# Performance work log

Hardware: AMD Instinct MI355X
Metric: run time of the kernel (lower is better)

The kernel has to match this reference:

```python
import jax, jax.numpy as jnp
import numpy as np

B, E, F = 16384, 128, 6
ITEM_V, CATE_V, HIST = 91718, 11, 50
I_IDX, J_IDX = np.triu_indices(F, k=1)  # 15 field pairs, loop order (0,1),(0,2),...
EPS = 1e-5


def _xavier(key, shape):
    fan_in, fan_out = shape[0], shape[-1]
    std = (2.0 / (fan_in + fan_out)) ** 0.5
    return std * jax.random.normal(key, shape, dtype=jnp.float32)


def setup_inputs() -> dict:
    key = jax.random.key(0)
    ks = jax.random.split(key, 20)
    inp = {
        'item_id': jax.random.randint(ks[0], (B,), 0, ITEM_V),
        'item_emb_d128': jax.random.normal(ks[1], (B, 128), dtype=jnp.float32),
        'likes_level': jax.random.randint(ks[2], (B,), 0, CATE_V),
        'views_level': jax.random.randint(ks[3], (B,), 0, CATE_V),
        'item_seq': jax.random.randint(ks[4], (B, HIST), 0, ITEM_V),
        # learned parameters
        'item_emb': 0.05 * jax.random.normal(ks[5], (ITEM_V, E), dtype=jnp.float32),
        'cate_emb': 0.05 * jax.random.normal(ks[6], (CATE_V, E), dtype=jnp.float32),
        'mm_W': _xavier(ks[7], (128, E)), 'mm_b': jnp.zeros((E,), jnp.float32),
        'ln_g': jnp.ones((E,), jnp.float32), 'ln_b': jnp.zeros((E,), jnp.float32),
        'se_W1': _xavier(ks[8], (F, F // 2)), 'se_b1': jnp.zeros((F // 2,), jnp.float32),
        'se_W2': _xavier(ks[9], (F // 2, F)), 'se_b2': jnp.zeros((F,), jnp.float32),
        'bi_W': _xavier(ks[10], (E, E)),
        'mlp_W1': _xavier(ks[11], (21 * E, 512)), 'mlp_b1': jnp.zeros((512,), jnp.float32),
        'bn1_g': jnp.ones((512,), jnp.float32), 'bn1_b': jnp.zeros((512,), jnp.float32),
        'bn1_rm': jnp.zeros((512,), jnp.float32), 'bn1_rv': jnp.ones((512,), jnp.float32),
        'mlp_W2': _xavier(ks[12], (512, 256)), 'mlp_b2': jnp.zeros((256,), jnp.float32),
        'bn2_g': jnp.ones((256,), jnp.float32), 'bn2_b': jnp.zeros((256,), jnp.float32),
        'bn2_rm': jnp.zeros((256,), jnp.float32), 'bn2_rv': jnp.ones((256,), jnp.float32),
        'mlp_W3': _xavier(ks[13], (256, 1)), 'mlp_b3': jnp.zeros((1,), jnp.float32),
    }
    return inp


def _forward(item_id, item_emb_d128, likes_level, views_level, item_seq,
             item_emb, cate_emb, mm_W, mm_b, ln_g, ln_b,
             se_W1, se_b1, se_W2, se_b2, bi_W,
             mlp_W1, mlp_b1, bn1_g, bn1_b, bn1_rm, bn1_rv,
             mlp_W2, mlp_b2, bn2_g, bn2_b, bn2_rm, bn2_rv,
             mlp_W3, mlp_b3):
    b = item_id.shape[0]
    tab = item_emb.at[0].set(0.0)  # padding_idx=0
    like_feat = cate_emb[likes_level]
    view_feat = cate_emb[views_level]
    item_feat = tab[item_id]
    # mm_proj: Linear -> LayerNorm -> ReLU
    mm = item_emb_d128 @ mm_W + mm_b
    mu = mm.mean(-1, keepdims=True)
    var = jnp.var(mm, axis=-1, keepdims=True)
    mm = jax.nn.relu((mm - mu) / jnp.sqrt(var + EPS) * ln_g + ln_b)
    # masked mean pooling over history
    seq_emb = tab[item_seq]                               # (B, HIST, E)
    valid = (item_seq != 0).astype(seq_emb.dtype)
    seq_sum = (seq_emb * valid[..., None]).sum(1)
    cnt = jnp.clip(valid.sum(1, keepdims=True), 1.0)
    hist_feat = seq_sum / cnt
    user_feat = jnp.zeros((b, E), seq_emb.dtype)
    x = jnp.stack([user_feat, like_feat, view_feat, item_feat, mm, hist_feat], axis=1)  # (B,6,E)
    # SENet
    z = x.mean(-1)
    w = jax.nn.sigmoid(jax.nn.relu(z @ se_W1 + se_b1) @ se_W2 + se_b2)
    xs = x * w[:, :, None]
    # bilinear 'all'
    xw = jnp.einsum('bfe,ed->bfd', xs, bi_W)
    p = xs[:, I_IDX, :] * xw[:, J_IDX, :]                 # (B,15,E)
    c = jnp.concatenate([xs.reshape(b, -1), p.reshape(b, -1)], axis=1)  # (B, 2688)
    # MLP head (eval mode: BN uses running stats, dropout off)
    h = c @ mlp_W1 + mlp_b1
    h = jax.nn.relu((h - bn1_rm) / jnp.sqrt(bn1_rv + EPS) * bn1_g + bn1_b)
    h = h @ mlp_W2 + mlp_b2
    h = jax.nn.relu((h - bn2_rm) / jnp.sqrt(bn2_rv + EPS) * bn2_g + bn2_b)
    logits = h @ mlp_W3 + mlp_b3
    return jax.nn.sigmoid(logits)[:, 0]


def reference(item_id, item_emb_d128, likes_level, views_level, item_seq,
              item_emb, cate_emb, mm_W, mm_b, ln_g, ln_b,
              se_W1, se_b1, se_W2, se_b2, bi_W,
              mlp_W1, mlp_b1, bn1_g, bn1_b, bn1_rm, bn1_rv,
              mlp_W2, mlp_b2, bn2_g, bn2_b, bn2_rm, bn2_rv,
              mlp_W3, mlp_b3):
    return _forward(item_id, item_emb_d128, likes_level, views_level, item_seq,
                    item_emb, cate_emb, mm_W, mm_b, ln_g, ln_b,
                    se_W1, se_b1, se_W2, se_b2, bi_W,
                    mlp_W1, mlp_b1, bn1_g, bn1_b, bn1_rm, bn1_rv,
                    mlp_W2, mlp_b2, bn2_g, bn2_b, bn2_rm, bn2_rv,
                    mlp_W3, mlp_b3)
```

## Files before the change

### kernel.cpp

```cpp
#include <hip/hip_runtime.h>
#include <hip/hip_bf16.h>

typedef __hip_bfloat16 bfloat;
typedef __bf16 bf16x8 __attribute__((ext_vector_type(8)));
typedef float f32x4 __attribute__((ext_vector_type(4)));

#define B_SZ   16384
#define E_DIM  128
#define HIST_L 50


#define IPACK 0x3221110000ULL
#define JPACK 0x3323213210ULL

__device__ __forceinline__ void gl_lds16(const void* g, void* l) {
    __builtin_amdgcn_global_load_lds(
        (const __attribute__((address_space(1))) unsigned int*)g,
        (__attribute__((address_space(3))) unsigned int*)l, 16, 0, 0);
}

__device__ __forceinline__ bf16x8 mul_bf16x8(bf16x8 a, bf16x8 b) {
    union { bf16x8 v; __hip_bfloat162 h[4]; } ua, ub, ur;
    ua.v = a; ub.v = b;
    #pragma unroll
    for (int i = 0; i < 4; ++i) ur.h[i] = __hmul2(ua.h[i], ub.h[i]);
    return ur.v;
}

__global__ __launch_bounds__(256) void feat_kernel(
    const int* __restrict__ item_id,
    const int* __restrict__ likes, const int* __restrict__ views,
    const int* __restrict__ seq,
    const float* __restrict__ item_emb, const float* __restrict__ cate_emb,
    const float* __restrict__ mm,
    const float* __restrict__ ln_g, const float* __restrict__ ln_b,
    const float* __restrict__ se_W1, const float* __restrict__ se_b1,
    const float* __restrict__ se_W2, const float* __restrict__ se_b2,
    bfloat* __restrict__ xs)
{
    const int tid = threadIdx.x;
    const int r   = tid >> 7;
    const int e   = tid & 127;
    const int b   = blockIdx.x * 2 + r;
    const int w   = tid >> 6;

    __shared__ float redh[2][4][128];
    __shared__ int   seq_s[2][64];
    __shared__ float lnred[4], lnred2[4];
    __shared__ float zred[5][4];
    __shared__ float wsh[2][6];
    __shared__ int   cnt_s[2];

    if (e < 64) seq_s[r][e] = (e < HIST_L) ? seq[(size_t)b * HIST_L + e] : 0;
    __syncthreads();

    const int iid = item_id[b];
    const float like_v = cate_emb[likes[b] * 128 + e];
    const float view_v = cate_emb[views[b] * 128 + e];
    const float item_raw = item_emb[(size_t)iid * 128 + e];
    const float item_v = iid ? item_raw : 0.f;
    const float acc = mm[(size_t)b * 128 + e];

    const int q   = e >> 5;
    const int l32 = e & 31;
    float4 hs = make_float4(0.f, 0.f, 0.f, 0.f);
    #pragma unroll
    for (int g = 0; g < 13; ++g) {
        int s = seq_s[r][g * 4 + q];
        const float4 v = *(const float4*)&item_emb[(size_t)s * 128 + l32 * 4];
        float m = (s != 0) ? 1.f : 0.f;
        hs.x = fmaf(v.x, m, hs.x);
        hs.y = fmaf(v.y, m, hs.y);
        hs.z = fmaf(v.z, m, hs.z);
        hs.w = fmaf(v.w, m, hs.w);
    }

    {
        float v = acc;
        #pragma unroll
        for (int off = 32; off > 0; off >>= 1) v += __shfl_down(v, off, 64);
        if ((tid & 63) == 0) lnred[w] = v;
    }
    __syncthreads();
    const float mu = (lnred[2 * r] + lnred[2 * r + 1]) * (1.f / 128.f);
    const float d  = acc - mu;
    {
        float v = d * d;
        #pragma unroll
        for (int off = 32; off > 0; off >>= 1) v += __shfl_down(v, off, 64);
        if ((tid & 63) == 0) lnred2[w] = v;
    }
    redh[r][q][l32 * 4 + 0] = hs.x;
    redh[r][q][l32 * 4 + 1] = hs.y;
    redh[r][q][l32 * 4 + 2] = hs.z;
    redh[r][q][l32 * 4 + 3] = hs.w;
    if ((w & 1) == 0 && e < 64) {
        bool valid = (e < HIST_L) && (seq_s[r][e] != 0);
        unsigned long long m = __ballot(valid);
        if (e == 0) cnt_s[r] = (int)__popcll(m);
    }
    __syncthreads();
    const float var = (lnred2[2 * r] + lnred2[2 * r + 1]) * (1.f / 128.f);
    float xmm = d * rsqrtf(var + 1e-5f) * ln_g[e] + ln_b[e];
    xmm = fmaxf(xmm, 0.f);

    const int cnt = cnt_s[r] > 0 ? cnt_s[r] : 1;
    const float hist_v = (redh[r][0][e] + redh[r][1][e] +
                          redh[r][2][e] + redh[r][3][e]) / (float)cnt;

    {
        float s1 = like_v, s2 = view_v, s3 = item_v, s4 = xmm, s5 = hist_v;
        #pragma unroll
        for (int off = 32; off > 0; off >>= 1) {
            s1 += __shfl_down(s1, off, 64);
            s2 += __shfl_down(s2, off, 64);
            s3 += __shfl_down(s3, off, 64);
            s4 += __shfl_down(s4, off, 64);
            s5 += __shfl_down(s5, off, 64);
        }
        if ((tid & 63) == 0) {
            zred[0][w] = s1; zred[1][w] = s2; zred[2][w] = s3;
            zred[3][w] = s4; zred[4][w] = s5;
        }
    }
    __syncthreads();

    if (e == 0) {
        float z[6];
        z[0] = 0.f;
        #pragma unroll
        for (int f = 1; f < 6; ++f)
            z[f] = (zred[f - 1][2 * r] + zred[f - 1][2 * r + 1]) * (1.f / 128.f);
        float a[3];
        #pragma unroll
        for (int j = 0; j < 3; ++j) {
            float s = se_b1[j];
            #pragma unroll
            for (int f = 0; f < 6; ++f) s += z[f] * se_W1[f * 3 + j];
            a[j] = fmaxf(s, 0.f);
        }
        #pragma unroll
        for (int f = 0; f < 6; ++f) {
            float s = se_b2[f];
            #pragma unroll
            for (int j = 0; j < 3; ++j) s += a[j] * se_W2[j * 6 + f];
            wsh[r][f] = 1.f / (1.f + expf(-s));
        }
    }
    __syncthreads();

    bfloat* xrow = xs + (size_t)b * 640;
    xrow[0 * 128 + e] = __float2bfloat16(like_v * wsh[r][1]);
    xrow[1 * 128 + e] = __float2bfloat16(view_v * wsh[r][2]);
    xrow[2 * 128 + e] = __float2bfloat16(item_v * wsh[r][3]);
    xrow[3 * 128 + e] = __float2bfloat16(xmm    * wsh[r][4]);
    xrow[4 * 128 + e] = __float2bfloat16(hist_v * wsh[r][5]);
}

__global__ __launch_bounds__(256) void transpose_f32_bf16(
    const float* __restrict__ in, bfloat* __restrict__ out, int K, int N)
{
    int idx = blockIdx.x * 256 + threadIdx.x;
    if (idx < K * N) {
        int k = idx / N, n = idx % N;
        out[(size_t)n * K + k] = __float2bfloat16(in[idx]);
    }
}

__global__ __launch_bounds__(256) void transpose_W1c(
    const float* __restrict__ W1, bfloat* __restrict__ W1t)
{
    int idx = blockIdx.x * 256 + threadIdx.x;
    if (idx < 512 * 1920) {
        int n = idx / 1920, kk = idx % 1920;
        int orig = kk + (kk < 640 ? 128 : 768);
        W1t[idx] = __float2bfloat16(W1[(size_t)orig * 512 + n]);
    }
}

__global__ __launch_bounds__(256) void cvt_f32_bf16(
    const float* __restrict__ in, bfloat* __restrict__ out, int n8)
{
    int idx = blockIdx.x * 256 + threadIdx.x;
    if (idx < n8) {
        float4 f0 = ((const float4*)in)[idx * 2];
        float4 f1 = ((const float4*)in)[idx * 2 + 1];
        union { bf16x8 v; unsigned short s[8]; } u;
        u.s[0] = __bfloat16_as_ushort(__float2bfloat16(f0.x));
        u.s[1] = __bfloat16_as_ushort(__float2bfloat16(f0.y));
        u.s[2] = __bfloat16_as_ushort(__float2bfloat16(f0.z));
        u.s[3] = __bfloat16_as_ushort(__float2bfloat16(f0.w));
        u.s[4] = __bfloat16_as_ushort(__float2bfloat16(f1.x));
        u.s[5] = __bfloat16_as_ushort(__float2bfloat16(f1.y));
        u.s[6] = __bfloat16_as_ushort(__float2bfloat16(f1.z));
        u.s[7] = __bfloat16_as_ushort(__float2bfloat16(f1.w));
        ((bf16x8*)out)[idx] = u.v;
    }
}

__global__ __launch_bounds__(256) void pair_kernel(
    const bfloat* __restrict__ xs, const bfloat* __restrict__ xw,
    bfloat* __restrict__ P, int total)
{
    int idx = blockIdx.x * 256 + threadIdx.x;
    if (idx >= total) return;
    int b = idx / 160, c = idx % 160;
    int pp = c >> 4, q = c & 15;
    int isl = (int)((IPACK >> (4 * pp)) & 15);
    int jsl = (int)((JPACK >> (4 * pp)) & 15);
    bf16x8 a = *(const bf16x8*)&xs[(size_t)b * 640 + isl * 128 + q * 8];
    bf16x8 w = *(const bf16x8*)&xw[((size_t)b * 4 + jsl) * 128 + q * 8];
    *(bf16x8*)&P[(size_t)b * 1280 + c * 8] = mul_bf16x8(a, w);
}

__global__ __launch_bounds__(256) void bn_pre(
    const float* __restrict__ lb1, const float* __restrict__ g1,
    const float* __restrict__ bb1, const float* __restrict__ rm1,
    const float* __restrict__ rv1,
    const float* __restrict__ lb2, const float* __restrict__ g2,
    const float* __restrict__ bb2, const float* __restrict__ rm2,
    const float* __restrict__ rv2,
    const float* __restrict__ mm_b,
    float* __restrict__ S1, float* __restrict__ T1,
    float* __restrict__ S2, float* __restrict__ T2,
    float* __restrict__ Tmm)
{
    int j = blockIdx.x * 256 + threadIdx.x;
    if (j < 512) {
        float s = g1[j] * rsqrtf(rv1[j] + 1e-5f);
        S1[j] = s;
        T1[j] = (lb1[j] - rm1[j]) * s + bb1[j];
    } else if (j < 768) {
        int k = j - 512;
        float s = g2[k] * rsqrtf(rv2[k] + 1e-5f);
        S2[k] = s;
        T2[k] = (lb2[k] - rm2[k]) * s + bb2[k];
    } else if (j < 896) {
        Tmm[j - 768] = mm_b[j - 768];
    }
}

template<int MODE, int EPI, int F32OUT>
__global__ __launch_bounds__(256) void gemm_bt(
    const void* __restrict__ A, const bfloat* __restrict__ A2,
    const bfloat* __restrict__ Bt, void* __restrict__ C,
    int M, int N, int K,
    const float* __restrict__ S, const float* __restrict__ T)
{
    __shared__ __align__(16) short As[3][64 * 64];
    __shared__ __align__(16) short Bs[3][64 * 64];

    const int tid  = threadIdx.x;
    const int bm   = blockIdx.x * 64;
    const int bn   = blockIdx.y * 64;
    const int wave = tid >> 6;
    const int lane = tid & 63;
    const int wm   = (wave >> 1) * 32;
    const int wn   = (wave & 1) * 32;

    const short* Ag  = (const short*)A;
    const short* A2g = (const short*)A2;
    const short* Bg  = (const short*)Bt;

    f32x4 acc[2][2];
    #pragma unroll
    for (int i = 0; i < 2; ++i)
        #pragma unroll
        for (int j = 0; j < 2; ++j)
            acc[i][j] = (f32x4){0.f, 0.f, 0.f, 0.f};

    const int srow = tid >> 3;
    const int sck  = tid & 7;

    auto stage = [&](int buf, int kt) {
        #pragma unroll
        for (int rr = 0; rr < 2; ++rr) {
            int row = srow + rr * 32;
            int g   = sck ^ (row & 7);
            gl_lds16(&Bg[(long)(bn + row) * K + kt + g * 8],
                     &Bs[buf][row * 64 + sck * 8]);
        }
        #pragma unroll
        for (int rr = 0; rr < 2; ++rr) {
            int row = srow + rr * 32;
            int g   = sck ^ (row & 7);
            const short* src;
            if (MODE == 4) {
                long rb = (long)(bm + row);
                src = (kt < 640)
                    ? &Ag [rb * 640  + kt + g * 8]
                    : &A2g[rb * 1280 + (kt - 640) + g * 8];
            } else if (MODE == 2) {
                int gr = bm + row;
                src = &Ag[((long)(gr >> 2)) * 640 +
                          ((gr & 3) + 1) * 128 + kt + g * 8];
            } else {
                src = &Ag[(long)(bm + row) * K + kt + g * 8];
            }
            gl_lds16(src, &As[buf][row * 64 + sck * 8]);
        }
    };

    const int rbase = lane & 15;
    const int cswz  = rbase & 7;

    const int nk = K >> 6;
    stage(0, 0);
    stage(1, 64);

    for (int i = 0; i < nk; ++i) {
        if (i + 1 < nk) asm volatile("s_waitcnt vmcnt(4)" ::: "memory");
        else            asm volatile("s_waitcnt vmcnt(0)" ::: "memory");
        __builtin_amdgcn_s_barrier();
        __builtin_amdgcn_sched_barrier(0);

        const int cur = i % 3;
        #pragma unroll
        for (int h = 0; h < 2; ++h) {
            const int cg = h * 4 + (lane >> 4);
            const int ca = (cg ^ cswz) << 3;
            bf16x8 af[2], bfr[2];
            #pragma unroll
            for (int mt = 0; mt < 2; ++mt)
                af[mt] = *(const bf16x8*)
                    &As[cur][(wm + mt * 16 + rbase) * 64 + ca];
            #pragma unroll
            for (int nt = 0; nt < 2; ++nt)
                bfr[nt] = *(const bf16x8*)
                    &Bs[cur][(wn + nt * 16 + rbase) * 64 + ca];
            #pragma unroll
            for (int mt = 0; mt < 2; ++mt)
                #pragma unroll
                for (int nt = 0; nt < 2; ++nt)
                    acc[mt][nt] = __builtin_amdgcn_mfma_f32_16x16x32_bf16(
                        af[mt], bfr[nt], acc[mt][nt], 0, 0, 0);
        }

        if (i + 2 < nk) stage((i + 2) % 3, (i + 2) << 6);
    }

    const int col0 = lane & 15;
    const int row0 = (lane >> 4) * 4;
    #pragma unroll
    for (int nt = 0; nt < 2; ++nt) {
        int col = bn + wn + nt * 16 + col0;
        float s = 1.f, t = 0.f;
        if (EPI) { s = (EPI == 1) ? S[col] : 1.f; t = T[col]; }
        #pragma unroll
        for (int mt = 0; mt < 2; ++mt) {
            #pragma unroll
            for (int i = 0; i < 4; ++i) {
                int row = bm + wm + mt * 16 + row0 + i;
                float v = acc[mt][nt][i];
                if (EPI == 1) v = fmaxf(v * s + t, 0.f);
                if (EPI == 2) v = v + t;
                if (F32OUT) ((float*)C)[(size_t)row * N + col] = v;
                else ((bfloat*)C)[(size_t)row * N + col] = __float2bfloat16(v);
            }
        }
    }
}

__global__ __launch_bounds__(256) void head_kernel(
    const bfloat* __restrict__ h2, const float* __restrict__ W3,
    const float* __restrict__ b3, float* __restrict__ out)
{
    int lane = threadIdx.x & 63;
    int row  = blockIdx.x * 4 + (threadIdx.x >> 6);
    float acc = 0.f;
    #pragma unroll
    for (int i = 0; i < 4; ++i)
        acc += __bfloat162float(h2[(size_t)row * 256 + i * 64 + lane]) *
               W3[i * 64 + lane];
    #pragma unroll
    for (int off = 32; off > 0; off >>= 1) acc += __shfl_down(acc, off, 64);
    if (lane == 0) {
        float l = acc + b3[0];
        out[row] = 1.f / (1.f + expf(-l));
    }
}

extern "C" void kernel_launch(void* const* d_in, const int* in_sizes, int n_in,
                              void* d_out, int out_size, void* d_ws, size_t ws_size,
                              hipStream_t stream) {
    const int*   item_id = (const int*)  d_in[0];
    const float* d128    = (const float*)d_in[1];
    const int*   likes   = (const int*)  d_in[2];
    const int*   views   = (const int*)  d_in[3];
    const int*   seq     = (const int*)  d_in[4];
    const float* item_emb= (const float*)d_in[5];
    const float* cate_emb= (const float*)d_in[6];
    const float* mm_W    = (const float*)d_in[7];
    const float* mm_b    = (const float*)d_in[8];
    const float* ln_g    = (const float*)d_in[9];
    const float* ln_b    = (const float*)d_in[10];
    const float* se_W1   = (const float*)d_in[11];
    const float* se_b1   = (const float*)d_in[12];
    const float* se_W2   = (const float*)d_in[13];
    const float* se_b2   = (const float*)d_in[14];
    const float* bi_W    = (const float*)d_in[15];
    const float* W1      = (const float*)d_in[16];
    const float* b1      = (const float*)d_in[17];
    const float* bn1_g   = (const float*)d_in[18];
    const float* bn1_b   = (const float*)d_in[19];
    const float* bn1_rm  = (const float*)d_in[20];
    const float* bn1_rv  = (const float*)d_in[21];
    const float* W2      = (const float*)d_in[22];
    const float* b2      = (const float*)d_in[23];
    const float* bn2_g   = (const float*)d_in[24];
    const float* bn2_b   = (const float*)d_in[25];
    const float* bn2_rm  = (const float*)d_in[26];
    const float* bn2_rv  = (const float*)d_in[27];
    const float* W3      = (const float*)d_in[28];
    const float* b3      = (const float*)d_in[29];

    const size_t fixed = 2300416;
    int CH = 1024;
    if      (fixed + (size_t)16384 * 5120 <= ws_size) CH = 16384;
    else if (fixed + (size_t)8192  * 5120 <= ws_size) CH = 8192;
    else if (fixed + (size_t)4096  * 5120 <= ws_size) CH = 4096;
    else if (fixed + (size_t)2048  * 5120 <= ws_size) CH = 2048;

    char* ws = (char*)d_ws;
    bfloat* W1t = (bfloat*)(ws);
    bfloat* W2t = (bfloat*)(ws + 1966080);
    bfloat* bWt = (bfloat*)(ws + 2228224);
    bfloat* mmWt= (bfloat*)(ws + 2260992);
    float*  S1  = (float*) (ws + 2293760);
    float*  T1  = (float*) (ws + 2295808);
    float*  S2  = (float*) (ws + 2297856);
    float*  T2  = (float*) (ws + 2298880);
    float*  Tmm = (float*) (ws + 2299904);
    bfloat* xs  = (bfloat*)(ws + fixed);
    bfloat* xw  = (bfloat*)(ws + fixed + (size_t)CH * 1280);
    bfloat* h1  = xw;
    bfloat* P   = (bfloat*)(ws + fixed + (size_t)CH * 2304);
    float*  mm  = (float*)P;
    bfloat* h2  = (bfloat*)P;
    bfloat* d128b = (bfloat*)(ws + fixed + (size_t)CH * 4864);

    transpose_W1c<<<(512 * 1920 + 255) / 256, 256, 0, stream>>>(W1, W1t);
    transpose_f32_bf16<<<(512 * 256 + 255) / 256, 256, 0, stream>>>(W2, W2t, 512, 256);
    transpose_f32_bf16<<<(128 * 128 + 255) / 256, 256, 0, stream>>>(bi_W, bWt, 128, 128);
    transpose_f32_bf16<<<(128 * 128 + 255) / 256, 256, 0, stream>>>(mm_W, mmWt, 128, 128);
    bn_pre<<<4, 256, 0, stream>>>(b1, bn1_g, bn1_b, bn1_rm, bn1_rv,
                                  b2, bn2_g, bn2_b, bn2_rm, bn2_rv,
                                  mm_b, S1, T1, S2, T2, Tmm);

    for (int off = 0; off < B_SZ; off += CH) {
        cvt_f32_bf16<<<(CH * 16 + 255) / 256, 256, 0, stream>>>(
            d128 + (size_t)off * 128, d128b, CH * 16);

        dim3 gmm(CH / 64, 2);
        gemm_bt<0, 2, 1><<<gmm, 256, 0, stream>>>(
            d128b, nullptr, mmWt, mm, CH, 128, 128, nullptr, Tmm);

        feat_kernel<<<CH / 2, 256, 0, stream>>>(
            item_id + off, likes + off, views + off,
            seq + (size_t)off * HIST_L, item_emb, cate_emb, mm,
            ln_g, ln_b, se_W1, se_b1, se_W2, se_b2, xs);

        dim3 gxw(CH * 4 / 64, 2);
        gemm_bt<2, 0, 0><<<gxw, 256, 0, stream>>>(
            xs, nullptr, bWt, xw, CH * 4, 128, 128, nullptr, nullptr);

        pair_kernel<<<(CH * 160 + 255) / 256, 256, 0, stream>>>(
            xs, xw, P, CH * 160);

        dim3 g1(CH / 64, 8);
        gemm_bt<4, 1, 0><<<g1, 256, 0, stream>>>(
            xs, P, W1t, h1, CH, 512, 1920, S1, T1);

        dim3 g2(CH / 64, 4);
        gemm_bt<0, 1, 0><<<g2, 256, 0, stream>>>(
            h1, nullptr, W2t, h2, CH, 256, 512, S2, T2);

        head_kernel<<<CH / 4, 256, 0, stream>>>(h2, W3, b3, (float*)d_out + off);
    }
}
```

Baseline: 314.6 us.

## Convert item embedding table to bf16 once and gather history from it

Adds a pass that converts the whole item embedding table to bf16 in the workspace, zeroing row 0 so the padding mask can be dropped. The feature kernel then gathers the 50-item history and the item row from the bf16 table, halving gather bytes. The workspace layout is also reshuffled so d128b and mm share the P region, and the batch chunk is capped at 8192. The one-off conversion reads all 47MB of the table on every call and lowers the precision of the gathered embeddings.

```diff
diff --git a/kernel.cpp b/kernel.cpp
--- a/kernel.cpp
+++ b/kernel.cpp
@@ -27,11 +27,12 @@
     return ur.v;
 }
 
+template<int TB>
 __global__ __launch_bounds__(256) void feat_kernel(
     const int* __restrict__ item_id,
     const int* __restrict__ likes, const int* __restrict__ views,
     const int* __restrict__ seq,
-    const float* __restrict__ item_emb, const float* __restrict__ cate_emb,
+    const void* __restrict__ item_tab, const float* __restrict__ cate_emb,
     const float* __restrict__ mm,
     const float* __restrict__ ln_g, const float* __restrict__ ln_b,
     const float* __restrict__ se_W1, const float* __restrict__ se_b1,
@@ -57,22 +58,43 @@
     const int iid = item_id[b];
     const float like_v = cate_emb[likes[b] * 128 + e];
     const float view_v = cate_emb[views[b] * 128 + e];
-    const float item_raw = item_emb[(size_t)iid * 128 + e];
-    const float item_v = iid ? item_raw : 0.f;
+    float item_v;
+    if (TB) {
+        const bfloat* tb = (const bfloat*)item_tab;
+        item_v = __bfloat162float(tb[(size_t)iid * 128 + e]);
+    } else {
+        const float* tf = (const float*)item_tab;
+        float raw = tf[(size_t)iid * 128 + e];
+        item_v = iid ? raw : 0.f;
+    }
     const float acc = mm[(size_t)b * 128 + e];
 
     const int q   = e >> 5;
     const int l32 = e & 31;
     float4 hs = make_float4(0.f, 0.f, 0.f, 0.f);
-    #pragma unroll
-    for (int g = 0; g < 13; ++g) {
-        int s = seq_s[r][g * 4 + q];
-        const float4 v = *(const float4*)&item_emb[(size_t)s * 128 + l32 * 4];
-        float m = (s != 0) ? 1.f : 0.f;
-        hs.x = fmaf(v.x, m, hs.x);
-        hs.y = fmaf(v.y, m, hs.y);
-        hs.z = fmaf(v.z, m, hs.z);
-        hs.w = fmaf(v.w, m, hs.w);
+    if (TB) {
+        const ushort* tb = (const ushort*)item_tab;
+        #pragma unroll
+        for (int g = 0; g < 13; ++g) {
+            int s = seq_s[r][g * 4 + q];
+            ushort4 v = *(const ushort4*)&tb[(size_t)s * 128 + l32 * 4];
+            hs.x += __bfloat162float(__ushort_as_bfloat16(v.x));
+            hs.y += __bfloat162float(__ushort_as_bfloat16(v.y));
+            hs.z += __bfloat162float(__ushort_as_bfloat16(v.z));
+            hs.w += __bfloat162float(__ushort_as_bfloat16(v.w));
+        }
+    } else {
+        const float* tf = (const float*)item_tab;
+        #pragma unroll
+        for (int g = 0; g < 13; ++g) {
+            int s = seq_s[r][g * 4 + q];
+            const float4 v = *(const float4*)&tf[(size_t)s * 128 + l32 * 4];
+            float m = (s != 0) ? 1.f : 0.f;
+            hs.x = fmaf(v.x, m, hs.x);
+            hs.y = fmaf(v.y, m, hs.y);
+            hs.z = fmaf(v.z, m, hs.z);
+            hs.w = fmaf(v.w, m, hs.w);
+        }
     }
 
     {
@@ -196,6 +218,32 @@
         u.s[7] = __bfloat16_as_ushort(__float2bfloat16(f1.w));
         ((bf16x8*)out)[idx] = u.v;
     }
+}
+
+__global__ __launch_bounds__(256) void cvt_emb(
+    const float* __restrict__ in, bfloat* __restrict__ out, int n8)
+{
+    int idx = blockIdx.x * 256 + threadIdx.x;
+    if (idx >= n8) return;
+    if (idx < 16) {
+        union { bf16x8 v; unsigned short s[8]; } z;
+        #pragma unroll
+        for (int i = 0; i < 8; ++i) z.s[i] = 0;
+        ((bf16x8*)out)[idx] = z.v;
+        return;
+    }
+    float4 f0 = ((const float4*)in)[idx * 2];
+    float4 f1 = ((const float4*)in)[idx * 2 + 1];
+    union { bf16x8 v; unsigned short s[8]; } u;
+    u.s[0] = __bfloat16_as_ushort(__float2bfloat16(f0.x));
+    u.s[1] = __bfloat16_as_ushort(__float2bfloat16(f0.y));
+    u.s[2] = __bfloat16_as_ushort(__float2bfloat16(f0.z));
+    u.s[3] = __bfloat16_as_ushort(__float2bfloat16(f0.w));
+    u.s[4] = __bfloat16_as_ushort(__float2bfloat16(f1.x));
+    u.s[5] = __bfloat16_as_ushort(__float2bfloat16(f1.y));
+    u.s[6] = __bfloat16_as_ushort(__float2bfloat16(f1.z));
+    u.s[7] = __bfloat16_as_ushort(__float2bfloat16(f1.w));
+    ((bf16x8*)out)[idx] = u.v;
 }
 
 __global__ __launch_bounds__(256) void pair_kernel(
@@ -415,11 +463,14 @@
     const float* b3      = (const float*)d_in[29];
 
     const size_t fixed = 2300416;
-    int CH = 1024;
-    if      (fixed + (size_t)16384 * 5120 <= ws_size) CH = 16384;
-    else if (fixed + (size_t)8192  * 5120 <= ws_size) CH = 8192;
-    else if (fixed + (size_t)4096  * 5120 <= ws_size) CH = 4096;
-    else if (fixed + (size_t)2048  * 5120 <= ws_size) CH = 2048;
+    const size_t ITB   = 23479808;
+    int CH; bool use_tb;
+    if      (fixed + ITB + (size_t)8192 * 4864 <= ws_size) { CH = 8192; use_tb = true;  }
+    else if (fixed + ITB + (size_t)4096 * 4864 <= ws_size) { CH = 4096; use_tb = true;  }
+    else if (fixed + (size_t)8192 * 4864 <= ws_size)       { CH = 8192; use_tb = false; }
+    else if (fixed + (size_t)4096 * 4864 <= ws_size)       { CH = 4096; use_tb = false; }
+    else if (fixed + (size_t)2048 * 4864 <= ws_size)       { CH = 2048; use_tb = false; }
+    else                                                   { CH = 1024; use_tb = false; }
 
     char* ws = (char*)d_ws;
     bfloat* W1t = (bfloat*)(ws);
@@ -431,13 +482,15 @@
     float*  S2  = (float*) (ws + 2297856);
     float*  T2  = (float*) (ws + 2298880);
     float*  Tmm = (float*) (ws + 2299904);
-    bfloat* xs  = (bfloat*)(ws + fixed);
-    bfloat* xw  = (bfloat*)(ws + fixed + (size_t)CH * 1280);
+    bfloat* itemb = (bfloat*)(ws + fixed);
+    char*   cb  = ws + fixed + (use_tb ? ITB : 0);
+    bfloat* xs  = (bfloat*)(cb);
+    bfloat* xw  = (bfloat*)(cb + (size_t)CH * 1280);
     bfloat* h1  = xw;
-    bfloat* P   = (bfloat*)(ws + fixed + (size_t)CH * 2304);
-    float*  mm  = (float*)P;
+    bfloat* P   = (bfloat*)(cb + (size_t)CH * 2304);
+    bfloat* d128b = (bfloat*)P;
+    float*  mm  = (float*)((char*)P + (size_t)CH * 256);
     bfloat* h2  = (bfloat*)P;
-    bfloat* d128b = (bfloat*)(ws + fixed + (size_t)CH * 4864);
 
     transpose_W1c<<<(512 * 1920 + 255) / 256, 256, 0, stream>>>(W1, W1t);
     transpose_f32_bf16<<<(512 * 256 + 255) / 256, 256, 0, stream>>>(W2, W2t, 512, 256);
@@ -446,6 +499,10 @@
     bn_pre<<<4, 256, 0, stream>>>(b1, bn1_g, bn1_b, bn1_rm, bn1_rv,
                                   b2, bn2_g, bn2_b, bn2_rm, bn2_rv,
                                   mm_b, S1, T1, S2, T2, Tmm);
+    if (use_tb) {
+        const int n8 = 91718 * 128 / 8;
+        cvt_emb<<<(n8 + 255) / 256, 256, 0, stream>>>(item_emb, itemb, n8);
+    }
 
     for (int off = 0; off < B_SZ; off += CH) {
         cvt_f32_bf16<<<(CH * 16 + 255) / 256, 256, 0, stream>>>(
@@ -455,10 +512,16 @@
         gemm_bt<0, 2, 1><<<gmm, 256, 0, stream>>>(
             d128b, nullptr, mmWt, mm, CH, 128, 128, nullptr, Tmm);
 
-        feat_kernel<<<CH / 2, 256, 0, stream>>>(
-            item_id + off, likes + off, views + off,
-            seq + (size_t)off * HIST_L, item_emb, cate_emb, mm,
-            ln_g, ln_b, se_W1, se_b1, se_W2, se_b2, xs);
+        if (use_tb)
+            feat_kernel<1><<<CH / 2, 256, 0, stream>>>(
+                item_id + off, likes + off, views + off,
+                seq + (size_t)off * HIST_L, itemb, cate_emb, mm,
+                ln_g, ln_b, se_W1, se_b1, se_W2, se_b2, xs);
+        else
+            feat_kernel<0><<<CH / 2, 256, 0, stream>>>(
+                item_id + off, likes + off, views + off,
+                seq + (size_t)off * HIST_L, item_emb, cate_emb, mm,
+                ln_g, ln_b, se_W1, se_b1, se_W2, se_b2, xs);
 
         dim3 gxw(CH * 4 / 64, 2);
         gemm_bt<2, 0, 0><<<gxw, 256, 0, stream>>>(
```

New measurement: 333.9 us. 1.06x slower.
